# Optimization experiments

Measured on AMD Instinct MI355X. Metric: run time of the kernel, lower is better.

Reference implementation:

```python
import jax, jax.numpy as jnp
from jax import lax
import numpy as np

# --- config (mirrors init_kwargs) ---
SCALES = (0.5, 1.0, 2.0)
RATIOS = (0.5, 1.0, 2.0)
MAX_DETECTIONS = 100
SCORE_THRESHOLD = 0.5
IOU_THRESHOLD = 0.75
PRE_NMS_TOPK = 1000          # candidates kept before O(K^2) NMS
ANCHOR_BASE_CELLS = 4.0      # anchor base size in grid cells
NEG_INF = -1e30


def create_anchors(grid_h, grid_w):
    """Anchors in normalized ijhw (center_i, center_j, h, w). -> [gh*gw*A, 4]"""
    ci = (jnp.arange(grid_h, dtype=jnp.float32) + 0.5) / grid_h
    cj = (jnp.arange(grid_w, dtype=jnp.float32) + 0.5) / grid_w
    s = jnp.asarray(SCALES, jnp.float32)
    r = jnp.asarray(RATIOS, jnp.float32)
    ss, rr = jnp.meshgrid(s, r, indexing='ij')          # [3,3]
    ah = (ss * jnp.sqrt(rr)).reshape(-1) * (ANCHOR_BASE_CELLS / grid_h)  # [A]
    aw = (ss / jnp.sqrt(rr)).reshape(-1) * (ANCHOR_BASE_CELLS / grid_w)  # [A]
    A = ah.shape[0]
    ii = jnp.broadcast_to(ci[:, None, None], (grid_h, grid_w, A))
    jj = jnp.broadcast_to(cj[None, :, None], (grid_h, grid_w, A))
    hh = jnp.broadcast_to(ah[None, None, :], (grid_h, grid_w, A))
    ww = jnp.broadcast_to(aw[None, None, :], (grid_h, grid_w, A))
    return jnp.stack([ii, jj, hh, ww], axis=-1).reshape(-1, 4)


def decode(t, anchors):
    """unmatch_fn: offsets -> absolute ijhw boxes. t: [..., N, C], anchors: [N, 4]."""
    ai, aj, ah, aw = anchors[:, 0], anchors[:, 1], anchors[:, 2], anchors[:, 3]
    di = ai + t[..., 0] * ah
    dj = aj + t[..., 1] * aw
    dh = ah * jnp.exp(t[..., 2])
    dw = aw * jnp.exp(t[..., 3])
    boxes = jnp.stack([di, dj, dh, dw], axis=-1)
    return jnp.concatenate([boxes, t[..., 4:]], axis=-1)


def ijhw_to_ijkl(b):
    """center ijhw -> corner ijkl."""
    i, j, h, w = b[..., 0], b[..., 1], b[..., 2], b[..., 3]
    return jnp.stack([i - h / 2, j - w / 2, i + h / 2, j + w / 2], axis=-1)


def iou_matrix(boxes):
    """boxes [K,4] ijkl -> pairwise IoU [K,K]."""
    a, b = boxes[:, None, :], boxes[None, :, :]
    ti = jnp.maximum(a[..., 0], b[..., 0])
    tj = jnp.maximum(a[..., 1], b[..., 1])
    bi = jnp.minimum(a[..., 2], b[..., 2])
    bj = jnp.minimum(a[..., 3], b[..., 3])
    inter = jnp.clip(bi - ti, 0.0) * jnp.clip(bj - tj, 0.0)
    area = (boxes[:, 2] - boxes[:, 0]) * (boxes[:, 3] - boxes[:, 1])
    union = area[:, None] + area[None, :] - inter
    return inter / jnp.maximum(union, 1e-12)


def nms_per_image(det):
    """det: [N, C]; returns [MAX_DETECTIONS, 6] = (i, j, h, w, label, score), zero-padded."""
    scores = det[:, 5]
    masked = jnp.where(scores >= SCORE_THRESHOLD, scores, NEG_INF)
    top_scores, idx = lax.top_k(masked, PRE_NMS_TOPK)        # score-sorted candidates
    cand = det[idx]                                          # [K, C]
    valid = top_scores > NEG_INF / 2
    iou = iou_matrix(ijhw_to_ijkl(cand[:, :4]))              # [K, K]
    K = PRE_NMS_TOPK
    col = jnp.arange(K)

    def body(suppressed, xs):
        iou_row, valid_i, i = xs
        keep_i = valid_i & ~suppressed[i]
        suppressed = suppressed | (keep_i & (iou_row > IOU_THRESHOLD) & (col > i))
        return suppressed, keep_i

    _, keep = lax.scan(body, jnp.zeros(K, bool), (iou, valid, col))
    # stable sort: kept candidates first, preserving score order
    order = jnp.argsort(jnp.where(keep, 0, 1))[:MAX_DETECTIONS]
    kept = keep[order]
    sel = cand[order]                                        # [MAX_DET, C]
    coords = sel[:, :4]
    score = sel[:, 5:6]
    labels = jnp.argmax(sel[:, 6:], axis=-1).astype(jnp.float32)[:, None]
    out = jnp.concatenate([coords, labels, score], axis=-1)  # [MAX_DET, 6]
    return jnp.where(kept[:, None], out, 0.0)                # fix_tensor_length padding


def setup_inputs() -> dict:
    key = jax.random.key(0)
    inputs = jax.random.normal(key, (8, 128, 128, 9, 86), dtype=jnp.float32)
    return {"inputs": inputs}


def reference(inputs) -> jnp.ndarray:
    b, gh, gw, na, c = inputs.shape
    anchors = create_anchors(gh, gw)                  # [gh*gw*na, 4]
    flat = inputs.reshape(b, gh * gw * na, c)
    det = decode(flat, anchors)                       # [b, N, c]
    return jax.vmap(nms_per_image)(det)               # [b, MAX_DETECTIONS, 6]
```

## Files before the change

kernel.cpp:

```cpp
#include <hip/hip_runtime.h>
#include <cstdint>
#include <cstddef>

typedef unsigned int u32;
typedef unsigned long long u64;

#define NB 8
#define GH 128
#define GW 128
#define NA 9
#define NC 86
#define NANCH (GH*GW*NA)
#define BLOCKS_PER_IMG (NANCH/256)
#define TOPK 1000
#define KCAP 1024
#define CANDCAP 2048
#define VALIDCAP 65536
#define HBINS 1024
#define HBASE 48896u

#define OFF_HIST      ((size_t)0)
#define SZ_HIST       ((size_t)NB*HBINS*4)
#define OFF_VCNT      (OFF_HIST + SZ_HIST)
#define OFF_CCNT      (OFF_VCNT + 32)
#define MEMSET_BYTES  (OFF_CCNT + 32)
#define OFF_CUT       (MEMSET_BYTES)
#define OFF_M         (OFF_CUT + 32)
#define OFF_VBUF      (OFF_M + 32)
#define SZ_VBUF       ((size_t)NB*VALIDCAP*8)
#define OFF_CBUF      (OFF_VBUF + SZ_VBUF)
#define SZ_CBUF       ((size_t)NB*CANDCAP*8)
#define OFF_DET       (OFF_CBUF + SZ_CBUF)
#define SZ_DET        ((size_t)NB*KCAP*8*4)
#define OFF_COR       (OFF_DET + SZ_DET)
#define SZ_COR        ((size_t)NB*KCAP*16)
#define OFF_AREA      (OFF_COR + SZ_COR)
#define SZ_AREA       ((size_t)NB*KCAP*4)
#define OFF_MASK      (OFF_AREA + SZ_AREA)
#define SZ_MASK       ((size_t)NB*KCAP*16*8)

__device__ __forceinline__ u64 shfl64(u64 v, int src) {
    int lo = __shfl((int)(v & 0xffffffffull), src, 64);
    int hi = __shfl((int)(v >> 32), src, 64);
    return ((u64)(u32)hi << 32) | (u32)lo;
}
__device__ __forceinline__ u64 shfl64_xor(u64 v, int m) {
    int lo = __shfl_xor((int)(v & 0xffffffffull), m, 64);
    int hi = __shfl_xor((int)(v >> 32), m, 64);
    return ((u64)(u32)hi << 32) | (u32)lo;
}
__device__ __forceinline__ u64 readlane64(u64 v, int lane) {
    int lo = __builtin_amdgcn_readlane((int)(v & 0xffffffffull), lane);
    int hi = __builtin_amdgcn_readlane((int)(v >> 32), lane);
    return ((u64)(u32)hi << 32) | (u32)lo;
}

__global__ __launch_bounds__(256) void k1_hist(const float* __restrict__ in,
                        u32* __restrict__ hist,
                        int* __restrict__ vcnt, u64* __restrict__ vbuf) {
    __shared__ int wcnt[4];
    __shared__ int woff[4];
    __shared__ int blockbase;
    int gid = blockIdx.x * 256 + threadIdx.x;
    int b = blockIdx.x / BLOCKS_PER_IMG;
    int lane = threadIdx.x & 63;
    int wv = threadIdx.x >> 6;
    float sc = in[(size_t)gid * NC + 5];
    bool valid = (sc >= 0.5f);
    u32 key = 0;
    if (valid) {
        key = __float_as_uint(sc) ^ 0x80000000u;
        u32 bin = key >> 16;
        if (bin < HBASE) bin = HBASE;
        if (bin > HBASE + HBINS - 1) bin = HBASE + HBINS - 1;
        atomicAdd(&hist[(b << 10) + (bin - HBASE)], 1u);
    }
    u64 mask = __ballot(valid);
    if (lane == 0) wcnt[wv] = __popcll(mask);
    __syncthreads();
    if (threadIdx.x == 0) {
        int c0 = wcnt[0], c1 = wcnt[1], c2 = wcnt[2], c3 = wcnt[3];
        woff[0] = 0; woff[1] = c0; woff[2] = c0 + c1; woff[3] = c0 + c1 + c2;
        blockbase = atomicAdd(&vcnt[b], c0 + c1 + c2 + c3);
    }
    __syncthreads();
    if (valid) {
        int prefix = __popcll(mask & ((1ull << lane) - 1ull));
        int p = blockbase + woff[wv] + prefix;
        u32 n = (u32)(gid - b * NANCH);
        if (p < VALIDCAP) vbuf[((size_t)b << 16) + p] = ((u64)key << 32) | (u32)(~n);
    }
}

__global__ __launch_bounds__(256) void k2_cut(const u32* __restrict__ hist,
                                              int* __restrict__ cut) {
    __shared__ u32 psum[256];
    int b = blockIdx.x, t = threadIdx.x;
    const u32* h = hist + (b << 10);
    int base = HBINS - 4 * (t + 1);
    psum[t] = h[base] + h[base + 1] + h[base + 2] + h[base + 3];
    __syncthreads();
    if (t == 0) {
        u32 cumv = 0; int res = 0; bool found = false;
        for (int c = 0; c < 256 && !found; ++c) {
            u32 cs = psum[c];
            if (cumv + cs >= (u32)TOPK) {
                int top = HBINS - 4 * c - 1;
                for (int i = top; i > top - 4; --i) {
                    cumv += h[i];
                    if (cumv >= (u32)TOPK) { res = i; found = true; break; }
                }
            } else cumv += cs;
        }
        cut[b] = found ? (res + (int)HBASE) : 0;
    }
}

__global__ __launch_bounds__(256) void k3_gather(const u64* __restrict__ vbuf,
                          const int* __restrict__ vcnt,
                          const int* __restrict__ cut, int* __restrict__ ccnt,
                          u64* __restrict__ cbuf) {
    __shared__ int wcnt[4];
    __shared__ int woff[4];
    __shared__ int blockbase;
    int gid = blockIdx.x * 256 + threadIdx.x;
    int b = gid >> 16, i = gid & 0xffff;
    int lane = threadIdx.x & 63;
    int wv = threadIdx.x >> 6;
    int cnt = vcnt[b]; if (cnt > VALIDCAP) cnt = VALIDCAP;
    bool take = false; u64 comp = 0;
    if (i < cnt) {
        comp = vbuf[((size_t)b << 16) + i];
        take = ((u32)(comp >> 48) >= (u32)cut[b]);
    }
    u64 mask = __ballot(take);
    if (lane == 0) wcnt[wv] = __popcll(mask);
    __syncthreads();
    if (threadIdx.x == 0) {
        int c0 = wcnt[0], c1 = wcnt[1], c2 = wcnt[2], c3 = wcnt[3];
        woff[0] = 0; woff[1] = c0; woff[2] = c0 + c1; woff[3] = c0 + c1 + c2;
        blockbase = (c0 + c1 + c2 + c3) ? atomicAdd(&ccnt[b], c0 + c1 + c2 + c3) : 0;
    }
    __syncthreads();
    if (take) {
        int p = blockbase + woff[wv] + __popcll(mask & ((1ull << lane) - 1ull));
        if (p < CANDCAP) cbuf[b * CANDCAP + p] = comp;
    }
}

__global__ __launch_bounds__(1024) void k4_sort(u64* __restrict__ cbuf,
                                                const int* __restrict__ ccnt,
                                                int* __restrict__ Mb) {
    __shared__ u64 buf[CANDCAP];
    int b = blockIdx.x, t = threadIdx.x;
    int cnt = ccnt[b]; if (cnt > CANDCAP) cnt = CANDCAP;
    buf[t]        = (t        < cnt) ? cbuf[b * CANDCAP + t]        : 0ull;
    buf[t + 1024] = (t + 1024 < cnt) ? cbuf[b * CANDCAP + t + 1024] : 0ull;
    __syncthreads();
    for (int k = 2; k <= CANDCAP; k <<= 1)
        for (int j = k >> 1; j > 0; j >>= 1) {
            int i = ((t & ~(j - 1)) << 1) | (t & (j - 1));
            int l = i | j;
            u64 a = buf[i], c = buf[l];
            bool up = ((i & k) == 0);
            if (up ? (a < c) : (a > c)) { buf[i] = c; buf[l] = a; }
            __syncthreads();
        }
    if (t < KCAP) cbuf[b * CANDCAP + t] = buf[t];
    if (t == 0) Mb[b] = cnt < TOPK ? cnt : TOPK;
}

__global__ void k5_decode(const float* __restrict__ in, const u64* __restrict__ cbuf,
                          const int* __restrict__ Mb, float* __restrict__ det,
                          float4* __restrict__ cor, float* __restrict__ area) {
    int gid = blockIdx.x * blockDim.x + threadIdx.x;
    int b = gid >> 10, k = gid & 1023;
    if (b >= NB) return;
    if (k >= Mb[b]) return;
    u64 comp = cbuf[b * CANDCAP + k];
    u32 idx = ~(u32)comp;
    int a = idx % 9; int cell = idx / 9;
    int gj = cell & 127, gi = cell >> 7;
    float ci = (gi + 0.5f) * (1.0f / GH);
    float cj = (gj + 0.5f) * (1.0f / GW);
    const float SCL[3] = {0.5f, 1.0f, 2.0f};
    float s = SCL[a / 3], r = SCL[a % 3];
    float sq = sqrtf(r);
    float ah = (s * sq) * (4.0f / GH);
    float aw = (s / sq) * (4.0f / GW);
    const float* row = in + ((size_t)b * NANCH + idx) * NC;
    float t0 = row[0], t1 = row[1], t2 = row[2], t3 = row[3], scv = row[5];
    float di = ci + t0 * ah;
    float dj = cj + t1 * aw;
    float dh = ah * expf(t2);
    float dw = aw * expf(t3);
    float i0 = di - dh * 0.5f, j0 = dj - dw * 0.5f;
    float i1 = di + dh * 0.5f, j1 = dj + dw * 0.5f;
    float best = row[6]; int lab = 0;
    for (int c = 1; c < 80; ++c) { float v = row[6 + c]; if (v > best) { best = v; lab = c; } }
    float* d = det + (size_t)(b * KCAP + k) * 8;
    d[0] = di; d[1] = dj; d[2] = dh; d[3] = dw; d[4] = (float)lab; d[5] = scv;
    cor[b * KCAP + k] = make_float4(i0, j0, i1, j1);
    area[b * KCAP + k] = (i1 - i0) * (j1 - j0);
}

__global__ __launch_bounds__(256) void k6_mask(const float4* __restrict__ cor,
                        const float* __restrict__ area,
                        const int* __restrict__ Mb, u64* __restrict__ mask) {
    __shared__ float4 scor[KCAP];
    __shared__ float sarea[KCAP];
    int b = blockIdx.x >> 8;
    int i = ((blockIdx.x & 255) << 2) + (threadIdx.x >> 6);
    int lane = threadIdx.x & 63;
    int m = Mb[b];
    for (int idx = threadIdx.x; idx < KCAP; idx += 256) {
        scor[idx] = cor[b * KCAP + idx];
        sarea[idx] = area[b * KCAP + idx];
    }
    __syncthreads();
    if (i >= m) return;
    float4 bi = scor[i]; float ai = sarea[i];
    u64* rowp = mask + ((size_t)(b * KCAP + i)) * 16;
    for (int w = 0; w < 16; ++w) {
        int j = w * 64 + lane;
        bool pred = false;
        if (j > i && j < m) {
            float4 bj = scor[j]; float aj = sarea[j];
            float ti = fmaxf(bi.x, bj.x), tj = fmaxf(bi.y, bj.y);
            float b2 = fminf(bi.z, bj.z), b3 = fminf(bi.w, bj.w);
            float inter = fmaxf(b2 - ti, 0.0f) * fmaxf(b3 - tj, 0.0f);
            float uni = (ai + aj) - inter;
            float iou = inter / fmaxf(uni, 1e-12f);
            pred = iou > 0.75f;
        }
        u64 word = __ballot(pred);
        if (lane == w) rowp[w] = word;
    }
}

__global__ __launch_bounds__(128) void k78_scan_out(const u64* __restrict__ mask,
                        const int* __restrict__ Mb, const float* __restrict__ det,
                        float* __restrict__ out) {
    __shared__ u64 kw[16];
    __shared__ int cum[17];
    int b = blockIdx.x, t = threadIdx.x;
    int m = Mb[b];
    if (t < 64) {
        int lane = t;
        const u64* mk = mask + (size_t)b * KCAP * 16;
        int myw = lane & 15;
        int myq = lane >> 4;
        u64 supp = 0;
        u64 colW = (lane < m) ? mk[(size_t)lane * 16 + 0] : 0ull;
        for (int g = 0; g < 16; ++g) {
            u64 rowW = colW;
            if (g + 1 < 16) {
                int rn = (g + 1) * 64 + lane;
                colW = (rn < m) ? mk[(size_t)rn * 16 + (g + 1)] : 0ull;
            }
            u64 cur = shfl64(supp, g);
            int lim = m - g * 64;
            u64 keptW = 0;
            #pragma unroll
            for (int s = 0; s < 64; ++s) {
                u64 w = readlane64(rowW, s);
                bool kept = (s < lim) && !((cur >> s) & 1ull);
                if (kept) { keptW |= (1ull << s); cur |= w; }
            }
            if (lane == 0) kw[g] = keptW;
            u64 acc = 0;
            #pragma unroll
            for (int s = 0; s < 16; ++s) {
                int r = myq * 16 + s;
                if ((keptW >> r) & 1ull)
                    acc |= mk[(size_t)(g * 64 + r) * 16 + myw];
            }
            acc |= shfl64_xor(acc, 16);
            acc |= shfl64_xor(acc, 32);
            if (lane < 16) supp |= acc;
        }
    }
    __syncthreads();
    if (t == 0) {
        int c = 0;
        for (int w = 0; w < 16; ++w) { cum[w] = c; c += __builtin_popcountll(kw[w]); }
        cum[16] = c;
    }
    __syncthreads();
    int total = cum[16];
    if (t < 100) {
        float o0 = 0, o1 = 0, o2 = 0, o3 = 0, o4 = 0, o5 = 0;
        if (t < total) {
            int w = 0;
            while (w < 15 && cum[w + 1] <= t) w++;
            int j = t - cum[w];
            u64 word = kw[w];
            for (int q = 0; q < j; ++q) word &= word - 1;
            int pos = __builtin_ctzll(word);
            int c = w * 64 + pos;
            const float* d = det + (size_t)(b * KCAP + c) * 8;
            o0 = d[0]; o1 = d[1]; o2 = d[2]; o3 = d[3]; o4 = d[4]; o5 = d[5];
        }
        float* op = out + (size_t)b * 600 + (size_t)t * 6;
        op[0] = o0; op[1] = o1; op[2] = o2; op[3] = o3; op[4] = o4; op[5] = o5;
    }
}

extern "C" void kernel_launch(void* const* d_in, const int* in_sizes, int n_in,
                              void* d_out, int out_size, void* d_ws, size_t ws_size,
                              hipStream_t stream) {
    const float* in = (const float*)d_in[0];
    float* out = (float*)d_out;
    char* ws = (char*)d_ws;
    u32* hist  = (u32*)(ws + OFF_HIST);
    int* vcnt  = (int*)(ws + OFF_VCNT);
    int* ccnt  = (int*)(ws + OFF_CCNT);
    int* cut   = (int*)(ws + OFF_CUT);
    int* Mb    = (int*)(ws + OFF_M);
    u64* vbuf  = (u64*)(ws + OFF_VBUF);
    u64* cbuf  = (u64*)(ws + OFF_CBUF);
    float* det = (float*)(ws + OFF_DET);
    float4* cor = (float4*)(ws + OFF_COR);
    float* area = (float*)(ws + OFF_AREA);
    u64* mask  = (u64*)(ws + OFF_MASK);

    hipMemsetAsync(ws, 0, MEMSET_BYTES, stream);
    k1_hist  <<<(NB * NANCH) / 256, 256, 0, stream>>>(in, hist, vcnt, vbuf);
    k2_cut   <<<NB, 256, 0, stream>>>(hist, cut);
    k3_gather<<<(NB * VALIDCAP) / 256, 256, 0, stream>>>(vbuf, vcnt, cut, ccnt, cbuf);
    k4_sort  <<<NB, 1024, 0, stream>>>(cbuf, ccnt, Mb);
    k5_decode<<<(NB * KCAP) / 256, 256, 0, stream>>>(in, cbuf, Mb, det, cor, area);
    k6_mask  <<<NB * 256, 256, 0, stream>>>(cor, area, Mb, mask);
    k78_scan_out<<<NB, 128, 0, stream>>>(mask, Mb, det, out);
}
```

Before: 659.4 us.

## Fuse cut, gather, sort and decode into one per-image kernel

Replaces four kernels (histogram cut search, global compaction, bitonic sort, decode) with one 1024-thread block per image. The cut is now found with a parallel suffix scan, candidates are compacted into shared memory through an LDS atomic counter, and sorted in place. Decode reads directly from shared memory. Barriers for bitonic strides under 64 are dropped on the assumption that a 64-wide wavefront runs in lockstep. This removes three launches and the global round-trips through cbuf, cut and ccnt. In exchange, the gather and decode phases run on only 8 blocks, which cuts parallelism. The skipped barriers also rely on wavefront-synchronous LDS behaviour.

```diff
diff --git a/kernel.cpp b/kernel.cpp
--- a/kernel.cpp
+++ b/kernel.cpp
@@ -92,116 +92,91 @@
     }
 }
 
-__global__ __launch_bounds__(256) void k2_cut(const u32* __restrict__ hist,
-                                              int* __restrict__ cut) {
-    __shared__ u32 psum[256];
+__global__ __launch_bounds__(1024) void k2345_cut_sort_decode(
+                        const float* __restrict__ in,
+                        const u32* __restrict__ hist,
+                        const u64* __restrict__ vbuf,
+                        const int* __restrict__ vcnt,
+                        int* __restrict__ Mb,
+                        float* __restrict__ det,
+                        float4* __restrict__ cor,
+                        float* __restrict__ area) {
+    __shared__ u64 buf[CANDCAP];
+    __shared__ int lcnt;
+    __shared__ u32 cutsh;
     int b = blockIdx.x, t = threadIdx.x;
-    const u32* h = hist + (b << 10);
-    int base = HBINS - 4 * (t + 1);
-    psum[t] = h[base] + h[base + 1] + h[base + 2] + h[base + 3];
-    __syncthreads();
-    if (t == 0) {
-        u32 cumv = 0; int res = 0; bool found = false;
-        for (int c = 0; c < 256 && !found; ++c) {
-            u32 cs = psum[c];
-            if (cumv + cs >= (u32)TOPK) {
-                int top = HBINS - 4 * c - 1;
-                for (int i = top; i > top - 4; --i) {
-                    cumv += h[i];
-                    if (cumv >= (u32)TOPK) { res = i; found = true; break; }
-                }
-            } else cumv += cs;
-        }
-        cut[b] = found ? (res + (int)HBASE) : 0;
-    }
-}
-
-__global__ __launch_bounds__(256) void k3_gather(const u64* __restrict__ vbuf,
-                          const int* __restrict__ vcnt,
-                          const int* __restrict__ cut, int* __restrict__ ccnt,
-                          u64* __restrict__ cbuf) {
-    __shared__ int wcnt[4];
-    __shared__ int woff[4];
-    __shared__ int blockbase;
-    int gid = blockIdx.x * 256 + threadIdx.x;
-    int b = gid >> 16, i = gid & 0xffff;
-    int lane = threadIdx.x & 63;
-    int wv = threadIdx.x >> 6;
+
+    u32* ssum = (u32*)buf;
+    ssum[t] = hist[(b << 10) + t];
+    if (t == 0) { lcnt = 0; cutsh = 0u; }
+    __syncthreads();
+    for (int off = 1; off < 1024; off <<= 1) {
+        u32 add = (t + off < 1024) ? ssum[t + off] : 0u;
+        __syncthreads();
+        ssum[t] += add;
+        __syncthreads();
+    }
+    u32 S = ssum[t];
+    u32 Sn = (t < 1023) ? ssum[t + 1] : 0u;
+    if (S >= (u32)TOPK && Sn < (u32)TOPK) cutsh = (u32)t + HBASE;
+    __syncthreads();
+    u32 cutv = cutsh;
+
     int cnt = vcnt[b]; if (cnt > VALIDCAP) cnt = VALIDCAP;
-    bool take = false; u64 comp = 0;
-    if (i < cnt) {
-        comp = vbuf[((size_t)b << 16) + i];
-        take = ((u32)(comp >> 48) >= (u32)cut[b]);
-    }
-    u64 mask = __ballot(take);
-    if (lane == 0) wcnt[wv] = __popcll(mask);
-    __syncthreads();
-    if (threadIdx.x == 0) {
-        int c0 = wcnt[0], c1 = wcnt[1], c2 = wcnt[2], c3 = wcnt[3];
-        woff[0] = 0; woff[1] = c0; woff[2] = c0 + c1; woff[3] = c0 + c1 + c2;
-        blockbase = (c0 + c1 + c2 + c3) ? atomicAdd(&ccnt[b], c0 + c1 + c2 + c3) : 0;
-    }
-    __syncthreads();
-    if (take) {
-        int p = blockbase + woff[wv] + __popcll(mask & ((1ull << lane) - 1ull));
-        if (p < CANDCAP) cbuf[b * CANDCAP + p] = comp;
-    }
-}
-
-__global__ __launch_bounds__(1024) void k4_sort(u64* __restrict__ cbuf,
-                                                const int* __restrict__ ccnt,
-                                                int* __restrict__ Mb) {
-    __shared__ u64 buf[CANDCAP];
-    int b = blockIdx.x, t = threadIdx.x;
-    int cnt = ccnt[b]; if (cnt > CANDCAP) cnt = CANDCAP;
-    buf[t]        = (t        < cnt) ? cbuf[b * CANDCAP + t]        : 0ull;
-    buf[t + 1024] = (t + 1024 < cnt) ? cbuf[b * CANDCAP + t + 1024] : 0ull;
-    __syncthreads();
+    for (int i = t; i < cnt; i += 1024) {
+        u64 comp = vbuf[((size_t)b << 16) + i];
+        if ((u32)(comp >> 48) >= cutv) {
+            int p = atomicAdd(&lcnt, 1);
+            if (p < CANDCAP) buf[p] = comp;
+        }
+    }
+    __syncthreads();
+    int M = lcnt; if (M > CANDCAP) M = CANDCAP;
+    if (t >= M) buf[t] = 0ull;
+    if (t + 1024 >= M) buf[t + 1024] = 0ull;
+    __syncthreads();
+
     for (int k = 2; k <= CANDCAP; k <<= 1)
         for (int j = k >> 1; j > 0; j >>= 1) {
+            if (j >= 64) __syncthreads();
             int i = ((t & ~(j - 1)) << 1) | (t & (j - 1));
             int l = i | j;
             u64 a = buf[i], c = buf[l];
             bool up = ((i & k) == 0);
             if (up ? (a < c) : (a > c)) { buf[i] = c; buf[l] = a; }
-            __syncthreads();
-        }
-    if (t < KCAP) cbuf[b * CANDCAP + t] = buf[t];
-    if (t == 0) Mb[b] = cnt < TOPK ? cnt : TOPK;
-}
-
-__global__ void k5_decode(const float* __restrict__ in, const u64* __restrict__ cbuf,
-                          const int* __restrict__ Mb, float* __restrict__ det,
-                          float4* __restrict__ cor, float* __restrict__ area) {
-    int gid = blockIdx.x * blockDim.x + threadIdx.x;
-    int b = gid >> 10, k = gid & 1023;
-    if (b >= NB) return;
-    if (k >= Mb[b]) return;
-    u64 comp = cbuf[b * CANDCAP + k];
-    u32 idx = ~(u32)comp;
-    int a = idx % 9; int cell = idx / 9;
-    int gj = cell & 127, gi = cell >> 7;
-    float ci = (gi + 0.5f) * (1.0f / GH);
-    float cj = (gj + 0.5f) * (1.0f / GW);
-    const float SCL[3] = {0.5f, 1.0f, 2.0f};
-    float s = SCL[a / 3], r = SCL[a % 3];
-    float sq = sqrtf(r);
-    float ah = (s * sq) * (4.0f / GH);
-    float aw = (s / sq) * (4.0f / GW);
-    const float* row = in + ((size_t)b * NANCH + idx) * NC;
-    float t0 = row[0], t1 = row[1], t2 = row[2], t3 = row[3], scv = row[5];
-    float di = ci + t0 * ah;
-    float dj = cj + t1 * aw;
-    float dh = ah * expf(t2);
-    float dw = aw * expf(t3);
-    float i0 = di - dh * 0.5f, j0 = dj - dw * 0.5f;
-    float i1 = di + dh * 0.5f, j1 = dj + dw * 0.5f;
-    float best = row[6]; int lab = 0;
-    for (int c = 1; c < 80; ++c) { float v = row[6 + c]; if (v > best) { best = v; lab = c; } }
-    float* d = det + (size_t)(b * KCAP + k) * 8;
-    d[0] = di; d[1] = dj; d[2] = dh; d[3] = dw; d[4] = (float)lab; d[5] = scv;
-    cor[b * KCAP + k] = make_float4(i0, j0, i1, j1);
-    area[b * KCAP + k] = (i1 - i0) * (j1 - j0);
+        }
+    __syncthreads();
+
+    int M2 = M < TOPK ? M : TOPK;
+    if (t == 0) Mb[b] = M2;
+
+    if (t < M2) {
+        u64 comp = buf[t];
+        u32 idx = ~(u32)comp;
+        int a = idx % 9; int cell = idx / 9;
+        int gj = cell & 127, gi = cell >> 7;
+        float ci = (gi + 0.5f) * (1.0f / GH);
+        float cj = (gj + 0.5f) * (1.0f / GW);
+        const float SCL[3] = {0.5f, 1.0f, 2.0f};
+        float s = SCL[a / 3], r = SCL[a % 3];
+        float sq = sqrtf(r);
+        float ah = (s * sq) * (4.0f / GH);
+        float aw = (s / sq) * (4.0f / GW);
+        const float* row = in + ((size_t)b * NANCH + idx) * NC;
+        float t0 = row[0], t1 = row[1], t2 = row[2], t3 = row[3], scv = row[5];
+        float di = ci + t0 * ah;
+        float dj = cj + t1 * aw;
+        float dh = ah * expf(t2);
+        float dw = aw * expf(t3);
+        float i0 = di - dh * 0.5f, j0 = dj - dw * 0.5f;
+        float i1 = di + dh * 0.5f, j1 = dj + dw * 0.5f;
+        float best = row[6]; int lab = 0;
+        for (int c = 1; c < 80; ++c) { float v = row[6 + c]; if (v > best) { best = v; lab = c; } }
+        float* d = det + (size_t)(b * KCAP + t) * 8;
+        d[0] = di; d[1] = dj; d[2] = dh; d[3] = dw; d[4] = (float)lab; d[5] = scv;
+        cor[b * KCAP + t] = make_float4(i0, j0, i1, j1);
+        area[b * KCAP + t] = (i1 - i0) * (j1 - j0);
+    }
 }
 
 __global__ __launch_bounds__(256) void k6_mask(const float4* __restrict__ cor,
@@ -314,11 +289,8 @@
     char* ws = (char*)d_ws;
     u32* hist  = (u32*)(ws + OFF_HIST);
     int* vcnt  = (int*)(ws + OFF_VCNT);
-    int* ccnt  = (int*)(ws + OFF_CCNT);
-    int* cut   = (int*)(ws + OFF_CUT);
     int* Mb    = (int*)(ws + OFF_M);
     u64* vbuf  = (u64*)(ws + OFF_VBUF);
-    u64* cbuf  = (u64*)(ws + OFF_CBUF);
     float* det = (float*)(ws + OFF_DET);
     float4* cor = (float4*)(ws + OFF_COR);
     float* area = (float*)(ws + OFF_AREA);
@@ -326,10 +298,7 @@
 
     hipMemsetAsync(ws, 0, MEMSET_BYTES, stream);
     k1_hist  <<<(NB * NANCH) / 256, 256, 0, stream>>>(in, hist, vcnt, vbuf);
-    k2_cut   <<<NB, 256, 0, stream>>>(hist, cut);
-    k3_gather<<<(NB * VALIDCAP) / 256, 256, 0, stream>>>(vbuf, vcnt, cut, ccnt, cbuf);
-    k4_sort  <<<NB, 1024, 0, stream>>>(cbuf, ccnt, Mb);
-    k5_decode<<<(NB * KCAP) / 256, 256, 0, stream>>>(in, cbuf, Mb, det, cor, area);
+    k2345_cut_sort_decode<<<NB, 1024, 0, stream>>>(in, hist, vbuf, vcnt, Mb, det, cor, area);
     k6_mask  <<<NB * 256, 256, 0, stream>>>(cor, area, Mb, mask);
     k78_scan_out<<<NB, 128, 0, stream>>>(mask, Mb, det, out);
 }
```

Measured after the change: 664.2 us. About the same (+0.7%).
